# Performance work log

Hardware: AMD Instinct MI355X
Metric: run time of the kernel (lower is better)

Reference implementation:

```python
import jax, jax.numpy as jnp
import numpy as np

V = 1_000_000        # max_id + 1
DIM = 128
B_PAIRS = 131072
NUM_NEGS = 8
B_IN = 65536


def _make_table(key):
    # tf.truncated_normal_initializer(stddev=1/sqrt(dim))
    std = 1.0 / (DIM ** 0.5)
    return jax.random.truncated_normal(key, -2.0, 2.0, (V, DIM), dtype=jnp.float32) * std


def setup_inputs() -> dict:
    key = jax.random.key(0)
    k1, k2, k3, k4, k5, k6 = jax.random.split(key, 6)
    return {
        "inputs": jax.random.randint(k1, (B_IN,), 0, V, dtype=jnp.int32),
        "src": jax.random.randint(k2, (B_PAIRS, 1), 0, V, dtype=jnp.int32),
        "pos": jax.random.randint(k3, (B_PAIRS, 1), 0, V, dtype=jnp.int32),
        "negs": jax.random.randint(k4, (B_PAIRS, NUM_NEGS), 0, V, dtype=jnp.int32),
        "target_table": _make_table(k5),
        "context_table": _make_table(k6),
    }


def reference(inputs, src, pos, negs, target_table, context_table):
    emb = target_table[src]            # [B, 1, D]
    emb_pos = context_table[pos]       # [B, 1, D]
    emb_negs = context_table[negs]     # [B, N, D]

    # decoder: per-pair dot products (batched matmul with transpose_b)
    logits = jnp.einsum("bid,bjd->bij", emb, emb_pos)        # [B, 1, 1]
    neg_logits = jnp.einsum("bid,bnd->bin", emb, emb_negs)   # [B, 1, N]

    # sigmoid_cross_entropy_with_logits: labels=1 -> softplus(-x); labels=0 -> softplus(x)
    loss = jnp.sum(jax.nn.softplus(-logits)) + jnp.sum(jax.nn.softplus(neg_logits))

    # mrr_score: positive placed last; ties broken toward negatives (lower index)
    ranks = 1 + jnp.sum(neg_logits >= logits, axis=-1)        # [B, 1]
    mrr = jnp.mean(1.0 / ranks.astype(jnp.float32))

    embedding = target_table[inputs]           # [B_IN, D]
    context_embedding = context_table[inputs]  # [B_IN, D]
    return embedding, context_embedding, loss, mrr
```

## Files before the change

kernel.cpp:

```cpp
#include <hip/hip_runtime.h>
#include <math.h>


constexpr int DIM  = 128;
constexpr int NNEG = 8;

__global__ __launch_bounds__(256) void gather_rows(
    const int*   __restrict__ inputs,
    const float* __restrict__ tgt,
    const float* __restrict__ ctx,
    float*       __restrict__ out_emb,
    float*       __restrict__ out_ctx,
    float*       __restrict__ scalars,
    int n_rows)
{
    if (blockIdx.x == 0 && threadIdx.x == 0) {
        scalars[0] = 0.0f;
        scalars[1] = 0.0f;
    }
    int tid = blockIdx.x * blockDim.x + threadIdx.x;
    if (tid < n_rows * 32) {
        int row  = tid >> 5;
        int lane = tid & 31;
        size_t idx = (size_t)inputs[row];
        const float4* s1 = (const float4*)(tgt + idx * DIM);
        const float4* s2 = (const float4*)(ctx + idx * DIM);
        ((float4*)(out_emb + (size_t)row * DIM))[lane] = s1[lane];
        ((float4*)(out_ctx + (size_t)row * DIM))[lane] = s2[lane];
    }
}

__global__ __launch_bounds__(256) void pair_loss(
    const int*   __restrict__ src,
    const int*   __restrict__ pos,
    const int*   __restrict__ negs,
    const float* __restrict__ tgt,
    const float* __restrict__ ctx,
    float*       __restrict__ scalars,
    int n_pairs,
    float inv_n)
{
    __shared__ float red[2 * 4];
    const int lane = threadIdx.x & 63;
    const int l16  = threadIdx.x & 15;
    const int gid  = (blockIdx.x * blockDim.x + threadIdx.x) >> 4;
    const int ngroups = (gridDim.x * blockDim.x) >> 4;

    float loss_acc = 0.0f;
    float mrr_acc  = 0.0f;

    for (int b = gid; b < n_pairs; b += ngroups) {
        int sidx = src[b];
        const float4* srow = (const float4*)(tgt + (size_t)sidx * DIM);
        float4 e0 = srow[l16 * 2 + 0];
        float4 e1 = srow[l16 * 2 + 1];

        int ci[1 + NNEG];
        ci[0] = pos[b];
        const int4* np = (const int4*)(negs + (size_t)b * NNEG);
        int4 n0 = np[0];
        int4 n1 = np[1];
        ci[1] = n0.x; ci[2] = n0.y; ci[3] = n0.z; ci[4] = n0.w;
        ci[5] = n1.x; ci[6] = n1.y; ci[7] = n1.z; ci[8] = n1.w;

        float dots[1 + NNEG];
#pragma unroll
        for (int c = 0; c < 1 + NNEG; ++c) {
            const float4* crow = (const float4*)(ctx + (size_t)ci[c] * DIM);
            float4 c0 = crow[l16 * 2 + 0];
            float4 c1 = crow[l16 * 2 + 1];
            float pa = e0.x * c0.x + e0.y * c0.y + e0.z * c0.z + e0.w * c0.w;
            float pb = e1.x * c1.x + e1.y * c1.y + e1.z * c1.z + e1.w * c1.w;
            float p  = pa + pb;
#pragma unroll
            for (int off = 8; off > 0; off >>= 1)
                p += __shfl_xor(p, off, 16);
            dots[c] = p;
        }

        float lg   = dots[0];
        float prod = 1.0f + __expf(-lg);
        int rank = 1;
#pragma unroll
        for (int n = 1; n <= NNEG; ++n) {
            prod *= 1.0f + __expf(dots[n]);
            rank += (dots[n] >= lg) ? 1 : 0;
        }
        loss_acc += __logf(prod);
        mrr_acc  += 1.0f / (float)rank;
    }

    float L = (l16 == 0) ? loss_acc : 0.0f;
    float M = (l16 == 0) ? mrr_acc  : 0.0f;
#pragma unroll
    for (int off = 32; off > 0; off >>= 1) {
        L += __shfl_xor(L, off);
        M += __shfl_xor(M, off);
    }
    const int wib = threadIdx.x >> 6;
    if (lane == 0) {
        red[wib * 2 + 0] = L;
        red[wib * 2 + 1] = M;
    }
    __syncthreads();
    if (threadIdx.x == 0) {
        float Ls = 0.0f, Ms = 0.0f;
#pragma unroll
        for (int w = 0; w < 4; ++w) { Ls += red[2 * w]; Ms += red[2 * w + 1]; }
        atomicAdd(&scalars[0], Ls);
        atomicAdd(&scalars[1], Ms * inv_n);
    }
}

extern "C" void kernel_launch(void* const* d_in, const int* in_sizes, int n_in,
                              void* d_out, int out_size, void* d_ws, size_t ws_size,
                              hipStream_t stream) {
    const int*   inputs = (const int*)d_in[0];
    const int*   src    = (const int*)d_in[1];
    const int*   pos    = (const int*)d_in[2];
    const int*   negs   = (const int*)d_in[3];
    const float* tgt    = (const float*)d_in[4];
    const float* ctx    = (const float*)d_in[5];

    const int b_in    = in_sizes[0];
    const int b_pairs = in_sizes[1];

    float* out      = (float*)d_out;
    float* out_emb  = out;
    float* out_ctx  = out + (size_t)b_in * DIM;
    float* scalars  = out + (size_t)2 * b_in * DIM;

    {
        int total  = b_in * 32;
        int blocks = (total + 255) / 256;
        gather_rows<<<blocks, 256, 0, stream>>>(inputs, tgt, ctx,
                                                out_emb, out_ctx, scalars, b_in);
    }
    {
        int blocks = 2048;
        float inv_n = 1.0f / (float)b_pairs;
        pair_loss<<<blocks, 256, 0, stream>>>(src, pos, negs, tgt, ctx,
                                              scalars, b_pairs, inv_n);
    }
}
```

Before: 133.9 us.

## Fuse gather and pair-loss kernels, use nontemporal copies and two-stage reduction

The row gather and the pair-loss computation now run in one grid-stride kernel, so the copy and the dot-product work can overlap on the GPU instead of running as two serialized launches. The gather copies use nontemporal loads and stores so the streamed output does not pollute the cache that the random context-table reads rely on. The global atomics are replaced by per-block partials in workspace plus a small single-block finalize kernel, which also removes the separate zeroing of the scalars. The cost is an extra launch, and the fused kernel with 2048 blocks may give the copy phase less parallelism than the old one-thread-per-float4 gather.

```diff
diff --git a/kernel.cpp b/kernel.cpp
--- a/kernel.cpp
+++ b/kernel.cpp
@@ -5,46 +5,43 @@
 constexpr int DIM  = 128;
 constexpr int NNEG = 8;
 
-__global__ __launch_bounds__(256) void gather_rows(
+typedef float f32x4 __attribute__((ext_vector_type(4)));
+
+__global__ __launch_bounds__(256) void fused(
     const int*   __restrict__ inputs,
-    const float* __restrict__ tgt,
-    const float* __restrict__ ctx,
-    float*       __restrict__ out_emb,
-    float*       __restrict__ out_ctx,
-    float*       __restrict__ scalars,
-    int n_rows)
-{
-    if (blockIdx.x == 0 && threadIdx.x == 0) {
-        scalars[0] = 0.0f;
-        scalars[1] = 0.0f;
-    }
-    int tid = blockIdx.x * blockDim.x + threadIdx.x;
-    if (tid < n_rows * 32) {
-        int row  = tid >> 5;
-        int lane = tid & 31;
-        size_t idx = (size_t)inputs[row];
-        const float4* s1 = (const float4*)(tgt + idx * DIM);
-        const float4* s2 = (const float4*)(ctx + idx * DIM);
-        ((float4*)(out_emb + (size_t)row * DIM))[lane] = s1[lane];
-        ((float4*)(out_ctx + (size_t)row * DIM))[lane] = s2[lane];
-    }
-}
-
-__global__ __launch_bounds__(256) void pair_loss(
     const int*   __restrict__ src,
     const int*   __restrict__ pos,
     const int*   __restrict__ negs,
     const float* __restrict__ tgt,
     const float* __restrict__ ctx,
-    float*       __restrict__ scalars,
-    int n_pairs,
-    float inv_n)
+    float*       __restrict__ out_emb,
+    float*       __restrict__ out_ctx,
+    float*       __restrict__ partials,
+    int b_in,
+    int n_pairs)
 {
-    __shared__ float red[2 * 4];
+    const int tid     = blockIdx.x * blockDim.x + threadIdx.x;
+    const int nthread = gridDim.x * blockDim.x;
+
+    {
+        const int total = b_in * 64;
+        for (int u = tid; u < total; u += nthread) {
+            int row   = u >> 6;
+            int sub   = u & 63;
+            int table = sub >> 5;
+            int lane  = sub & 31;
+            size_t idx = (size_t)inputs[row];
+            const f32x4* s = (const f32x4*)((table ? ctx : tgt) + idx * DIM);
+            f32x4 v = __builtin_nontemporal_load(s + lane);
+            f32x4* d = (f32x4*)((table ? out_ctx : out_emb) + (size_t)row * DIM);
+            __builtin_nontemporal_store(v, d + lane);
+        }
+    }
+
     const int lane = threadIdx.x & 63;
     const int l16  = threadIdx.x & 15;
-    const int gid  = (blockIdx.x * blockDim.x + threadIdx.x) >> 4;
-    const int ngroups = (gridDim.x * blockDim.x) >> 4;
+    const int gid  = tid >> 4;
+    const int ngroups = nthread >> 4;
 
     float loss_acc = 0.0f;
     float mrr_acc  = 0.0f;
@@ -97,6 +94,7 @@
         L += __shfl_xor(L, off);
         M += __shfl_xor(M, off);
     }
+    __shared__ float red[2 * 4];
     const int wib = threadIdx.x >> 6;
     if (lane == 0) {
         red[wib * 2 + 0] = L;
@@ -107,8 +105,40 @@
         float Ls = 0.0f, Ms = 0.0f;
 #pragma unroll
         for (int w = 0; w < 4; ++w) { Ls += red[2 * w]; Ms += red[2 * w + 1]; }
-        atomicAdd(&scalars[0], Ls);
-        atomicAdd(&scalars[1], Ms * inv_n);
+        partials[blockIdx.x * 2 + 0] = Ls;
+        partials[blockIdx.x * 2 + 1] = Ms;
+    }
+}
+
+__global__ __launch_bounds__(256) void finalize(
+    const float* __restrict__ partials,
+    float*       __restrict__ scalars,
+    int nblocks,
+    float inv_n)
+{
+    float L = 0.0f, M = 0.0f;
+    for (int i = threadIdx.x; i < nblocks; i += 256) {
+        L += partials[2 * i + 0];
+        M += partials[2 * i + 1];
+    }
+#pragma unroll
+    for (int off = 32; off > 0; off >>= 1) {
+        L += __shfl_xor(L, off);
+        M += __shfl_xor(M, off);
+    }
+    __shared__ float red[2 * 4];
+    const int wib = threadIdx.x >> 6;
+    if ((threadIdx.x & 63) == 0) {
+        red[wib * 2 + 0] = L;
+        red[wib * 2 + 1] = M;
+    }
+    __syncthreads();
+    if (threadIdx.x == 0) {
+        float Ls = 0.0f, Ms = 0.0f;
+#pragma unroll
+        for (int w = 0; w < 4; ++w) { Ls += red[2 * w]; Ms += red[2 * w + 1]; }
+        scalars[0] = Ls;
+        scalars[1] = Ms * inv_n;
     }
 }
 
@@ -129,17 +159,12 @@
     float* out_emb  = out;
     float* out_ctx  = out + (size_t)b_in * DIM;
     float* scalars  = out + (size_t)2 * b_in * DIM;
+    float* partials = (float*)d_ws;
 
-    {
-        int total  = b_in * 32;
-        int blocks = (total + 255) / 256;
-        gather_rows<<<blocks, 256, 0, stream>>>(inputs, tgt, ctx,
-                                                out_emb, out_ctx, scalars, b_in);
-    }
-    {
-        int blocks = 2048;
-        float inv_n = 1.0f / (float)b_pairs;
-        pair_loss<<<blocks, 256, 0, stream>>>(src, pos, negs, tgt, ctx,
-                                              scalars, b_pairs, inv_n);
-    }
+    const int blocks = 2048;
+    fused<<<blocks, 256, 0, stream>>>(inputs, src, pos, negs, tgt, ctx,
+                                      out_emb, out_ctx, partials,
+                                      b_in, b_pairs);
+    finalize<<<1, 256, 0, stream>>>(partials, scalars, blocks,
+                                    1.0f / (float)b_pairs);
 }
```

Result: faster. 126.2 us (-5.8%).
